# Optimization experiments

Hardware: AMD Instinct MI355X
Metric: run time of the kernel (lower is better)

## Reference

```python
import jax, jax.numpy as jnp
import numpy as np

N_NODES = 100000
N_EDGES = 3200000
DROP_P = 0.5


def gcn_conv(x, W, b, src, dst, deg_inv_sqrt, n):
    # PyG GCNConv with self-loops already folded into (src, dst):
    # out[j] = sum_{(i->j)} dinv[i]*dinv[j] * (x W)[i] + b
    h = x @ W
    norm = deg_inv_sqrt[src] * deg_inv_sqrt[dst]          # [E+N]
    msg = h[src] * norm[:, None]                          # [E+N, d_out]
    out = jax.ops.segment_sum(msg, dst, num_segments=n)
    return out + b


def dropout(x, key, p=DROP_P):
    keep = jax.random.bernoulli(key, 1.0 - p, x.shape)
    return jnp.where(keep, x / (1.0 - p), 0.0)


def setup_inputs() -> dict:
    key = jax.random.key(0)
    ks = jax.random.split(key, 8)
    x = jax.random.normal(ks[0], (N_NODES, 64), dtype=jnp.float32)
    edge_index = jax.random.randint(ks[1], (2, N_EDGES), 0, N_NODES, dtype=jnp.int64)
    def glorot(k, fin, fout):
        lim = float(np.sqrt(6.0 / (fin + fout)))
        return jax.random.uniform(k, (fin, fout), jnp.float32, -lim, lim)
    return {
        "x": x,
        "edge_index": edge_index,
        "W1": glorot(ks[2], 64, 32), "b1": jnp.zeros((32,), jnp.float32),
        "W2": glorot(ks[3], 32, 64), "b2": jnp.zeros((64,), jnp.float32),
        "W3": glorot(ks[4], 64, 32), "b3": jnp.zeros((32,), jnp.float32),
    }


def reference(x, edge_index, W1, b1, W2, b2, W3, b3):
    n = x.shape[0]
    loops = jnp.arange(n, dtype=edge_index.dtype)
    src = jnp.concatenate([edge_index[0], loops])          # [E+N]
    dst = jnp.concatenate([edge_index[1], loops])
    deg = jax.ops.segment_sum(jnp.ones_like(dst, dtype=x.dtype), dst, num_segments=n)
    deg_inv_sqrt = jnp.where(deg > 0, jax.lax.rsqrt(deg), 0.0)

    dkey = jax.random.key(42)
    k1, k2 = jax.random.split(dkey)

    h = gcn_conv(x, W1, b1, src, dst, deg_inv_sqrt, n)
    h = jax.nn.celu(h)
    h = dropout(h, k1)
    h = gcn_conv(h, W2, b2, src, dst, deg_inv_sqrt, n)
    h = jax.nn.celu(h)
    h = dropout(h, k2)
    h = gcn_conv(h, W3, b3, src, dst, deg_inv_sqrt, n)
    return jax.nn.celu(h)
```

## Files before the change

kernel.cpp:

```cpp
#include <hip/hip_runtime.h>
#include <stdint.h>
#include <stddef.h>

__host__ __device__ __forceinline__ uint32_t rotl32(uint32_t v, uint32_t r) {
  return (v << r) | (v >> (32u - r));
}

__host__ __device__ __forceinline__ void tf2x32(uint32_t k0, uint32_t k1,
                                                uint32_t x0, uint32_t x1,
                                                uint32_t& o0, uint32_t& o1) {
  uint32_t ks2 = k0 ^ k1 ^ 0x1BD11BDAu;
  x0 += k0; x1 += k1;
  x0 += x1; x1 = rotl32(x1, 13); x1 ^= x0;
  x0 += x1; x1 = rotl32(x1, 15); x1 ^= x0;
  x0 += x1; x1 = rotl32(x1, 26); x1 ^= x0;
  x0 += x1; x1 = rotl32(x1, 6);  x1 ^= x0;
  x0 += k1; x1 += ks2 + 1u;
  x0 += x1; x1 = rotl32(x1, 17); x1 ^= x0;
  x0 += x1; x1 = rotl32(x1, 29); x1 ^= x0;
  x0 += x1; x1 = rotl32(x1, 16); x1 ^= x0;
  x0 += x1; x1 = rotl32(x1, 24); x1 ^= x0;
  x0 += ks2; x1 += k0 + 2u;
  x0 += x1; x1 = rotl32(x1, 13); x1 ^= x0;
  x0 += x1; x1 = rotl32(x1, 15); x1 ^= x0;
  x0 += x1; x1 = rotl32(x1, 26); x1 ^= x0;
  x0 += x1; x1 = rotl32(x1, 6);  x1 ^= x0;
  x0 += k0; x1 += k1 + 3u;
  x0 += x1; x1 = rotl32(x1, 17); x1 ^= x0;
  x0 += x1; x1 = rotl32(x1, 29); x1 ^= x0;
  x0 += x1; x1 = rotl32(x1, 16); x1 ^= x0;
  x0 += x1; x1 = rotl32(x1, 24); x1 ^= x0;
  x0 += k1; x1 += ks2 + 4u;
  x0 += x1; x1 = rotl32(x1, 13); x1 ^= x0;
  x0 += x1; x1 = rotl32(x1, 15); x1 ^= x0;
  x0 += x1; x1 = rotl32(x1, 26); x1 ^= x0;
  x0 += x1; x1 = rotl32(x1, 6);  x1 ^= x0;
  x0 += ks2; x1 += k0 + 5u;
  o0 = x0; o1 = x1;
}

__device__ __forceinline__ bool tf_keep(uint32_t k0, uint32_t k1, uint32_t idx) {
  uint32_t o0, o1;
  tf2x32(k0, k1, 0u, idx, o0, o1);
  return ((o0 ^ o1) >> 31) == 0u;
}

#define CHUNK 4096
#define STASH 5120

__global__ __launch_bounds__(1024) void zero1024(uint32_t* __restrict__ p) {
  p[threadIdx.x] = 0u;
}

__global__ __launch_bounds__(256) void k1_hist(const int* __restrict__ dst,
                                               uint32_t* __restrict__ tbl,
                                               uint32_t* __restrict__ gbcnt,
                                               int E, int NB) {
  __shared__ uint32_t lc[1024];
  int tid = threadIdx.x;
  for (int i = tid; i < NB; i += 256) lc[i] = 0u;
  __syncthreads();
  int base = blockIdx.x * CHUNK;
  int end = min(base + CHUNK, E);
  for (int i = base + tid; i < end; i += 256)
    atomicAdd(&lc[((uint32_t)dst[i]) >> 7], 1u);
  __syncthreads();
  uint32_t* row = tbl + (size_t)blockIdx.x * NB;
  for (int i = tid; i < NB; i += 256) {
    uint32_t c = lc[i];
    row[i] = c;
    if (c) atomicAdd(&gbcnt[i], c);
  }
}

__global__ __launch_bounds__(1024) void k3_bscan(const uint32_t* __restrict__ gbcnt,
                                                 uint32_t* __restrict__ bbase, int NB) {
  __shared__ uint32_t s[1024];
  int i = threadIdx.x;
  uint32_t v = (i < NB) ? gbcnt[i] : 0u;
  s[i] = v;
  __syncthreads();
  for (int off = 1; off < 1024; off <<= 1) {
    uint32_t t = (i >= off) ? s[i - off] : 0u;
    __syncthreads();
    if (i >= off) s[i] += t;
    __syncthreads();
  }
  if (i < NB) bbase[i] = s[i] - v;
}

__global__ __launch_bounds__(256) void k4_bin(const int* __restrict__ src,
                                              const int* __restrict__ dst,
                                              uint32_t* __restrict__ tbl,
                                              uint32_t* __restrict__ staging,
                                              int E, int NB) {
  __shared__ uint32_t lcur[1024];
  __shared__ uint32_t ls[256];
  __shared__ uint32_t stage[CHUNK];
  int tid = threadIdx.x;
  uint32_t* row = tbl + (size_t)blockIdx.x * NB;
  uint32_t carry = 0u;
  for (int seg = 0; seg < 1024; seg += 256) {
    int i = seg + tid;
    uint32_t v = (i < NB) ? row[i] : 0u;
    ls[tid] = v;
    __syncthreads();
    for (int off = 1; off < 256; off <<= 1) {
      uint32_t t = (tid >= off) ? ls[tid - off] : 0u;
      __syncthreads();
      if (tid >= off) ls[tid] += t;
      __syncthreads();
    }
    uint32_t excl = carry + ls[tid] - v;
    if (i < NB) {
      row[i] = (excl << 16) | v;
      lcur[i] = excl;
    }
    carry += ls[255];
    __syncthreads();
  }
  int base = blockIdx.x * CHUNK;
  int end = min(base + CHUNK, E);
  for (int i = base + tid; i < end; i += 256) {
    uint32_t d = (uint32_t)dst[i];
    uint32_t b = d >> 7;
    uint32_t p = atomicAdd(&lcur[b], 1u);
    stage[p] = ((d & 127u) << 17) | (uint32_t)src[i];
  }
  __syncthreads();
  int cnt_total = end - base;
  uint32_t* outp = staging + (size_t)blockIdx.x * CHUNK;
  for (int i = tid; i < cnt_total; i += 256) outp[i] = stage[i];
}

__global__ __launch_bounds__(256) void k5_fin(
    const uint32_t* __restrict__ staging, const uint32_t* __restrict__ tbl,
    const uint32_t* __restrict__ bbase, uint32_t* __restrict__ rowp,
    float* __restrict__ dinv, uint32_t* __restrict__ esrc,
    int n, int E, int NBLK, int NB) {
  __shared__ uint32_t loff[1024];
  __shared__ uint32_t P[1025];
  __shared__ uint32_t ls[256];
  __shared__ uint32_t stash[STASH];
  __shared__ uint32_t lc[128];
  __shared__ uint32_t sc[128];
  __shared__ uint32_t lcur[128];
  int tid = threadIdx.x;
  int b = blockIdx.x;
  if (tid < 128) lc[tid] = 0u;
  uint32_t carry = 0u;
  for (int seg = 0; seg < 1024; seg += 256) {
    int i = seg + tid;
    uint32_t packed = (i < NBLK) ? tbl[(size_t)i * NB + b] : 0u;
    uint32_t v = packed & 0xFFFFu;
    if (i < 1024) loff[i] = packed >> 16;
    ls[tid] = v;
    __syncthreads();
    for (int off = 1; off < 256; off <<= 1) {
      uint32_t t = (tid >= off) ? ls[tid - off] : 0u;
      __syncthreads();
      if (tid >= off) ls[tid] += t;
      __syncthreads();
    }
    if (i < 1024) P[i] = carry + ls[tid] - v;
    carry += ls[255];
    __syncthreads();
  }
  if (tid == 0) P[NBLK] = carry;
  __syncthreads();
  uint32_t total = P[NBLK];
  for (uint32_t q = tid; q < total; q += 256) {
    int lo = 0, hi = NBLK;
    while (hi - lo > 1) {
      int mid = (lo + hi) >> 1;
      if (P[mid] <= q) lo = mid; else hi = mid;
    }
    uint32_t e = staging[(size_t)lo * CHUNK + loff[lo] + (q - P[lo])];
    if (q < STASH) stash[q] = e;
    atomicAdd(&lc[e >> 17], 1u);
  }
  __syncthreads();
  uint32_t myc = (tid < 128) ? lc[tid] : 0u;
  if (tid < 128) sc[tid] = myc;
  __syncthreads();
  for (int off = 1; off < 128; off <<= 1) {
    uint32_t t = (tid < 128 && tid >= off) ? sc[tid - off] : 0u;
    __syncthreads();
    if (tid < 128 && tid >= off) sc[tid] += t;
    __syncthreads();
  }
  uint32_t s = bbase[b];
  if (tid < 128) {
    uint32_t gstart = s + sc[tid] - myc;
    int node = (b << 7) + tid;
    if (node < n) {
      rowp[node] = gstart;
      dinv[node] = 1.0f / sqrtf((float)(myc + 1u));
    }
    lcur[tid] = gstart;
  }
  if (b == 0 && tid == 0) rowp[n] = (uint32_t)E;
  __syncthreads();
  for (uint32_t q = tid; q < total; q += 256) {
    uint32_t e;
    if (q < STASH) {
      e = stash[q];
    } else {
      int lo = 0, hi = NBLK;
      while (hi - lo > 1) {
        int mid = (lo + hi) >> 1;
        if (P[mid] <= q) lo = mid; else hi = mid;
      }
      e = staging[(size_t)lo * CHUNK + loff[lo] + (q - P[lo])];
    }
    uint32_t pos = atomicAdd(&lcur[e >> 17], 1u);
    esrc[pos] = e & 0x1FFFFu;
  }
}

__global__ __launch_bounds__(256) void gemm_n64_k32(
    const float* __restrict__ X, const float* __restrict__ W,
    const float* __restrict__ dinv, float* __restrict__ out, int n) {
  __shared__ float Ws[64 * 32];
  __shared__ float Xs[32 * 68];
  int tid = threadIdx.x;
  {
    const float4* Wv = (const float4*)W;
    float4* Wsv = (float4*)Ws;
    Wsv[tid] = Wv[tid];
    Wsv[tid + 256] = Wv[tid + 256];
  }
  int row0 = blockIdx.x * 32;
  {
    const float4* Xv = (const float4*)(X + (size_t)row0 * 64);
    int lim = (n - row0) * 16;
    float4 z = make_float4(0.f, 0.f, 0.f, 0.f);
    int i0 = tid, i1 = tid + 256;
    float4 v0 = (i0 < lim) ? Xv[i0] : z;
    float4 v1 = (i1 < lim) ? Xv[i1] : z;
    *(float4*)(Xs + (i0 >> 4) * 68 + ((i0 & 15) << 2)) = v0;
    *(float4*)(Xs + (i1 >> 4) * 68 + ((i1 & 15) << 2)) = v1;
  }
  __syncthreads();
  int r = tid >> 3;
  int c4 = (tid & 7) << 2;
  int row = row0 + r;
  if (row >= n) return;
  float4 acc = make_float4(0.f, 0.f, 0.f, 0.f);
#pragma unroll
  for (int k = 0; k < 64; k += 4) {
    float4 xv = *(const float4*)(Xs + r * 68 + k);
    float4 w0 = *(const float4*)(Ws + (k + 0) * 32 + c4);
    float4 w1 = *(const float4*)(Ws + (k + 1) * 32 + c4);
    float4 w2 = *(const float4*)(Ws + (k + 2) * 32 + c4);
    float4 w3 = *(const float4*)(Ws + (k + 3) * 32 + c4);
    acc.x = fmaf(xv.x, w0.x, acc.x); acc.y = fmaf(xv.x, w0.y, acc.y);
    acc.z = fmaf(xv.x, w0.z, acc.z); acc.w = fmaf(xv.x, w0.w, acc.w);
    acc.x = fmaf(xv.y, w1.x, acc.x); acc.y = fmaf(xv.y, w1.y, acc.y);
    acc.z = fmaf(xv.y, w1.z, acc.z); acc.w = fmaf(xv.y, w1.w, acc.w);
    acc.x = fmaf(xv.z, w2.x, acc.x); acc.y = fmaf(xv.z, w2.y, acc.y);
    acc.z = fmaf(xv.z, w2.z, acc.z); acc.w = fmaf(xv.z, w2.w, acc.w);
    acc.x = fmaf(xv.w, w3.x, acc.x); acc.y = fmaf(xv.w, w3.y, acc.y);
    acc.z = fmaf(xv.w, w3.z, acc.z); acc.w = fmaf(xv.w, w3.w, acc.w);
  }
  float dj = dinv[row];
  acc.x *= dj; acc.y *= dj; acc.z *= dj; acc.w *= dj;
  *(float4*)(out + (size_t)row * 32 + c4) = acc;
}

__global__ __launch_bounds__(256) void gemm_k32_n64_act(
    const float* __restrict__ X, const float* __restrict__ W,
    const float* __restrict__ bias, float* __restrict__ out,
    uint32_t k0, uint32_t k1, int n) {
  __shared__ float Ws[32 * 64];
  __shared__ float Xs[16 * 36];
  int tid = threadIdx.x;
  {
    const float4* Wv = (const float4*)W;
    float4* Wsv = (float4*)Ws;
    Wsv[tid] = Wv[tid];
    Wsv[tid + 256] = Wv[tid + 256];
  }
  int row0 = blockIdx.x * 16;
  if (tid < 128) {
    const float4* Xv = (const float4*)(X + (size_t)row0 * 32);
    int lim = (n - row0) * 8;
    float4 z = make_float4(0.f, 0.f, 0.f, 0.f);
    float4 v = (tid < lim) ? Xv[tid] : z;
    *(float4*)(Xs + (tid >> 3) * 36 + ((tid & 7) << 2)) = v;
  }
  __syncthreads();
  int r = tid >> 4;
  int c4 = (tid & 15) << 2;
  int row = row0 + r;
  if (row >= n) return;
  float4 acc = make_float4(0.f, 0.f, 0.f, 0.f);
#pragma unroll
  for (int k = 0; k < 32; k += 4) {
    float4 xv = *(const float4*)(Xs + r * 36 + k);
    float4 w0 = *(const float4*)(Ws + (k + 0) * 64 + c4);
    float4 w1 = *(const float4*)(Ws + (k + 1) * 64 + c4);
    float4 w2 = *(const float4*)(Ws + (k + 2) * 64 + c4);
    float4 w3 = *(const float4*)(Ws + (k + 3) * 64 + c4);
    acc.x = fmaf(xv.x, w0.x, acc.x); acc.y = fmaf(xv.x, w0.y, acc.y);
    acc.z = fmaf(xv.x, w0.z, acc.z); acc.w = fmaf(xv.x, w0.w, acc.w);
    acc.x = fmaf(xv.y, w1.x, acc.x); acc.y = fmaf(xv.y, w1.y, acc.y);
    acc.z = fmaf(xv.y, w1.z, acc.z); acc.w = fmaf(xv.y, w1.w, acc.w);
    acc.x = fmaf(xv.z, w2.x, acc.x); acc.y = fmaf(xv.z, w2.y, acc.y);
    acc.z = fmaf(xv.z, w2.z, acc.z); acc.w = fmaf(xv.z, w2.w, acc.w);
    acc.x = fmaf(xv.w, w3.x, acc.x); acc.y = fmaf(xv.w, w3.y, acc.y);
    acc.z = fmaf(xv.w, w3.z, acc.z); acc.w = fmaf(xv.w, w3.w, acc.w);
  }
  float4 bv = *(const float4*)(bias + c4);
  float vv[4] = {acc.x + bv.x, acc.y + bv.y, acc.z + bv.z, acc.w + bv.w};
  uint32_t base = (uint32_t)row * 64u + (uint32_t)c4;
#pragma unroll
  for (int q = 0; q < 4; ++q) {
    float v = vv[q];
    v = v > 0.f ? v : expm1f(v);
    vv[q] = tf_keep(k0, k1, base + q) ? v * 2.f : 0.f;
  }
  *(float4*)(out + (size_t)row * 64 + c4) = make_float4(vv[0], vv[1], vv[2], vv[3]);
}

__global__ __launch_bounds__(256) void gather_fin(
    const float* __restrict__ hs, const uint32_t* __restrict__ rowp,
    const uint32_t* __restrict__ esrc, const float* __restrict__ dinv,
    const float* __restrict__ bias, float* __restrict__ out,
    int n, int mode, uint32_t k0, uint32_t k1) {
  int gt = blockIdx.x * 256 + threadIdx.x;
  int j = gt >> 5;
  if (j >= n) return;
  int l = threadIdx.x & 31;
  int eslot = l >> 3;
  int c4 = (l & 7) << 2;
  float4 acc = make_float4(0.f, 0.f, 0.f, 0.f);
  uint32_t e1 = rowp[j + 1];
  uint32_t e = rowp[j] + (uint32_t)eslot;
  for (; e + 4 < e1; e += 8) {
    uint32_t s0 = esrc[e];
    uint32_t s1 = esrc[e + 4];
    float4 v0 = *(const float4*)(hs + ((size_t)s0 << 5) + c4);
    float4 v1 = *(const float4*)(hs + ((size_t)s1 << 5) + c4);
    acc.x += v0.x + v1.x;
    acc.y += v0.y + v1.y;
    acc.z += v0.z + v1.z;
    acc.w += v0.w + v1.w;
  }
  if (e < e1) {
    uint32_t s0 = esrc[e];
    float4 v0 = *(const float4*)(hs + ((size_t)s0 << 5) + c4);
    acc.x += v0.x; acc.y += v0.y; acc.z += v0.z; acc.w += v0.w;
  }
  acc.x += __shfl_xor(acc.x, 8);  acc.y += __shfl_xor(acc.y, 8);
  acc.z += __shfl_xor(acc.z, 8);  acc.w += __shfl_xor(acc.w, 8);
  acc.x += __shfl_xor(acc.x, 16); acc.y += __shfl_xor(acc.y, 16);
  acc.z += __shfl_xor(acc.z, 16); acc.w += __shfl_xor(acc.w, 16);
  int srcLane = (threadIdx.x & 32) | (l >> 2);
  float va = __shfl(acc.x, srcLane);
  float vb = __shfl(acc.y, srcLane);
  float vc = __shfl(acc.z, srcLane);
  float vd = __shfl(acc.w, srcLane);
  float lo = (l & 1) ? vb : va;
  float hi = (l & 1) ? vd : vc;
  float sum = (l & 2) ? hi : lo;
  sum += hs[gt];
  float dj = dinv[j];
  float v = dj * sum;
  if (mode == 1) {
    v += bias[l];
    v = v > 0.f ? v : expm1f(v);
  } else if (mode == 3) {
    v += bias[l];
    v = v > 0.f ? v : expm1f(v);
    v = tf_keep(k0, k1, (uint32_t)gt) ? v * 2.f : 0.f;
    v *= dj;
  }
  out[gt] = v;
}

extern "C" void kernel_launch(void* const* d_in, const int* in_sizes, int n_in,
                              void* d_out, int out_size, void* d_ws, size_t ws_size,
                              hipStream_t stream) {
  const float* x  = (const float*)d_in[0];
  const int*   ei = (const int*)d_in[1];
  const float* W1 = (const float*)d_in[2];
  const float* b1 = (const float*)d_in[3];
  const float* W2 = (const float*)d_in[4];
  const float* b2 = (const float*)d_in[5];
  const float* W3 = (const float*)d_in[6];
  const float* b3 = (const float*)d_in[7];
  float* out = (float*)d_out;

  const int n = in_sizes[0] / 64;
  const int E = in_sizes[1] / 2;
  const int* src = ei;
  const int* dst = ei + E;

  char* ws = (char*)d_ws;
  size_t off = 0;
  auto alloc = [&](size_t bytes) {
    void* p = ws + off;
    off = (off + bytes + 255) & ~(size_t)255;
    return p;
  };
  float*    A     = (float*)alloc((size_t)n * 32 * 4);
  float*    B     = (float*)alloc((size_t)n * 32 * 4);
  float*    C     = (float*)alloc((size_t)n * 64 * 4);
  float*    dinv  = (float*)alloc((size_t)n * 4);
  uint32_t* rowp  = (uint32_t*)alloc((size_t)(n + 1) * 4);
  uint32_t* esrc  = (uint32_t*)alloc((size_t)E * 4);
  uint32_t* gbcnt = (uint32_t*)alloc(1024 * 4);
  uint32_t* bbase = (uint32_t*)alloc(1024 * 4);
  uint32_t* staging = (uint32_t*)C;
  uint32_t* tbl     = (uint32_t*)A;
  (void)ws_size; (void)n_in; (void)out_size;

  uint32_t k1a, k1b, k2a, k2b;
  tf2x32(0u, 42u, 0u, 0u, k1a, k1b);
  tf2x32(0u, 42u, 0u, 1u, k2a, k2b);

  const int NB   = (n + 127) >> 7;
  const int NBLK = (E + CHUNK - 1) / CHUNK;
  const int nv   = n * 32;
  const int gV   = (nv + 255) / 256;
  const int gG1  = (n + 31) / 32;
  const int gG2  = (n + 15) / 16;
  dim3 blk(256);

  zero1024<<<1, dim3(1024), 0, stream>>>(gbcnt);
  k1_hist<<<NBLK, blk, 0, stream>>>(dst, tbl, gbcnt, E, NB);
  k3_bscan<<<1, dim3(1024), 0, stream>>>(gbcnt, bbase, NB);
  k4_bin<<<NBLK, blk, 0, stream>>>(src, dst, tbl, staging, E, NB);
  k5_fin<<<NB, blk, 0, stream>>>(staging, tbl, bbase, rowp, dinv, esrc, n, E, NBLK, NB);

  gemm_n64_k32<<<gG1, blk, 0, stream>>>(x, W1, dinv, A, n);
  gather_fin<<<gV, blk, 0, stream>>>(A, rowp, esrc, dinv, b1, B, n, 3, k1a, k1b);

  gather_fin<<<gV, blk, 0, stream>>>(B, rowp, esrc, dinv, nullptr, A, n, 0, 0u, 0u);
  gemm_k32_n64_act<<<gG2, blk, 0, stream>>>(A, W2, b2, C, k2a, k2b, n);

  gemm_n64_k32<<<gG1, blk, 0, stream>>>(C, W3, dinv, A, n);
  gather_fin<<<gV, blk, 0, stream>>>(A, rowp, esrc, dinv, b3, out, n, 1, 0u, 0u);
}
```

Measured before the change: 381.3 us.

## Fuse histogram and binning passes, drop binary search, cooperative index loads in gather

Merges the edge histogram and the binning kernel into one launch that keeps dst/src in registers, so the edge arrays are read once and one launch disappears. The CSR finalize kernel now walks each source block's run directly instead of binary-searching the prefix table per edge. The gather kernel loads 32 neighbour indices with one coalesced wavefront-wide read and broadcasts them by shuffle, instead of each lane reading indices separately. The trade-offs are higher register use in the fused kernel, and a per-thread serial run walk in finalize that can load-imbalance and lose coalescing.

```diff
diff --git a/kernel.cpp b/kernel.cpp
--- a/kernel.cpp
+++ b/kernel.cpp
@@ -52,25 +52,59 @@
   p[threadIdx.x] = 0u;
 }
 
-__global__ __launch_bounds__(256) void k1_hist(const int* __restrict__ dst,
-                                               uint32_t* __restrict__ tbl,
-                                               uint32_t* __restrict__ gbcnt,
-                                               int E, int NB) {
-  __shared__ uint32_t lc[1024];
+__global__ __launch_bounds__(256) void k4_binhist(const int* __restrict__ src,
+                                                  const int* __restrict__ dst,
+                                                  uint32_t* __restrict__ tbl,
+                                                  uint32_t* __restrict__ gbcnt,
+                                                  uint32_t* __restrict__ staging,
+                                                  int E, int NB) {
+  __shared__ uint32_t lcur[1024];
+  __shared__ uint32_t ls[256];
+  __shared__ uint32_t stage[CHUNK];
   int tid = threadIdx.x;
-  for (int i = tid; i < NB; i += 256) lc[i] = 0u;
+  for (int i = tid; i < NB; i += 256) lcur[i] = 0u;
   __syncthreads();
   int base = blockIdx.x * CHUNK;
   int end = min(base + CHUNK, E);
-  for (int i = base + tid; i < end; i += 256)
-    atomicAdd(&lc[((uint32_t)dst[i]) >> 7], 1u);
-  __syncthreads();
-  uint32_t* row = tbl + (size_t)blockIdx.x * NB;
-  for (int i = tid; i < NB; i += 256) {
-    uint32_t c = lc[i];
-    row[i] = c;
-    if (c) atomicAdd(&gbcnt[i], c);
-  }
+  uint32_t dv[16], sv[16];
+  int m = 0;
+  for (int i = base + tid; i < end; i += 256) {
+    dv[m] = (uint32_t)dst[i];
+    sv[m] = (uint32_t)src[i];
+    ++m;
+  }
+  for (int q = 0; q < m; ++q) atomicAdd(&lcur[dv[q] >> 7], 1u);
+  __syncthreads();
+  uint32_t carry = 0u;
+  for (int seg = 0; seg < 1024; seg += 256) {
+    int i = seg + tid;
+    uint32_t v = (i < NB) ? lcur[i] : 0u;
+    ls[tid] = v;
+    __syncthreads();
+    for (int off = 1; off < 256; off <<= 1) {
+      uint32_t t = (tid >= off) ? ls[tid - off] : 0u;
+      __syncthreads();
+      if (tid >= off) ls[tid] += t;
+      __syncthreads();
+    }
+    uint32_t excl = carry + ls[tid] - v;
+    if (i < NB) {
+      tbl[(size_t)blockIdx.x * NB + i] = (excl << 16) | v;
+      if (v) atomicAdd(&gbcnt[i], v);
+      lcur[i] = excl;
+    }
+    carry += ls[255];
+    __syncthreads();
+  }
+  for (int q = 0; q < m; ++q) {
+    uint32_t d = dv[q];
+    uint32_t p = atomicAdd(&lcur[d >> 7], 1u);
+    stage[p] = ((d & 127u) << 17) | sv[q];
+  }
+  __syncthreads();
+  int cnt_total = end - base;
+  uint32_t* outp = staging + (size_t)blockIdx.x * CHUNK;
+  for (int i = tid; i < cnt_total; i += 256) outp[i] = stage[i];
 }
 
 __global__ __launch_bounds__(1024) void k3_bscan(const uint32_t* __restrict__ gbcnt,
@@ -89,56 +123,12 @@
   if (i < NB) bbase[i] = s[i] - v;
 }
 
-__global__ __launch_bounds__(256) void k4_bin(const int* __restrict__ src,
-                                              const int* __restrict__ dst,
-                                              uint32_t* __restrict__ tbl,
-                                              uint32_t* __restrict__ staging,
-                                              int E, int NB) {
-  __shared__ uint32_t lcur[1024];
-  __shared__ uint32_t ls[256];
-  __shared__ uint32_t stage[CHUNK];
-  int tid = threadIdx.x;
-  uint32_t* row = tbl + (size_t)blockIdx.x * NB;
-  uint32_t carry = 0u;
-  for (int seg = 0; seg < 1024; seg += 256) {
-    int i = seg + tid;
-    uint32_t v = (i < NB) ? row[i] : 0u;
-    ls[tid] = v;
-    __syncthreads();
-    for (int off = 1; off < 256; off <<= 1) {
-      uint32_t t = (tid >= off) ? ls[tid - off] : 0u;
-      __syncthreads();
-      if (tid >= off) ls[tid] += t;
-      __syncthreads();
-    }
-    uint32_t excl = carry + ls[tid] - v;
-    if (i < NB) {
-      row[i] = (excl << 16) | v;
-      lcur[i] = excl;
-    }
-    carry += ls[255];
-    __syncthreads();
-  }
-  int base = blockIdx.x * CHUNK;
-  int end = min(base + CHUNK, E);
-  for (int i = base + tid; i < end; i += 256) {
-    uint32_t d = (uint32_t)dst[i];
-    uint32_t b = d >> 7;
-    uint32_t p = atomicAdd(&lcur[b], 1u);
-    stage[p] = ((d & 127u) << 17) | (uint32_t)src[i];
-  }
-  __syncthreads();
-  int cnt_total = end - base;
-  uint32_t* outp = staging + (size_t)blockIdx.x * CHUNK;
-  for (int i = tid; i < cnt_total; i += 256) outp[i] = stage[i];
-}
-
 __global__ __launch_bounds__(256) void k5_fin(
     const uint32_t* __restrict__ staging, const uint32_t* __restrict__ tbl,
     const uint32_t* __restrict__ bbase, uint32_t* __restrict__ rowp,
     float* __restrict__ dinv, uint32_t* __restrict__ esrc,
     int n, int E, int NBLK, int NB) {
-  __shared__ uint32_t loff[1024];
+  __shared__ uint32_t lpak[1024];
   __shared__ uint32_t P[1025];
   __shared__ uint32_t ls[256];
   __shared__ uint32_t stash[STASH];
@@ -152,8 +142,8 @@
   for (int seg = 0; seg < 1024; seg += 256) {
     int i = seg + tid;
     uint32_t packed = (i < NBLK) ? tbl[(size_t)i * NB + b] : 0u;
+    lpak[i] = packed;
     uint32_t v = packed & 0xFFFFu;
-    if (i < 1024) loff[i] = packed >> 16;
     ls[tid] = v;
     __syncthreads();
     for (int off = 1; off < 256; off <<= 1) {
@@ -162,22 +152,25 @@
       if (tid >= off) ls[tid] += t;
       __syncthreads();
     }
-    if (i < 1024) P[i] = carry + ls[tid] - v;
+    P[i] = carry + ls[tid] - v;
     carry += ls[255];
     __syncthreads();
   }
   if (tid == 0) P[NBLK] = carry;
   __syncthreads();
   uint32_t total = P[NBLK];
-  for (uint32_t q = tid; q < total; q += 256) {
-    int lo = 0, hi = NBLK;
-    while (hi - lo > 1) {
-      int mid = (lo + hi) >> 1;
-      if (P[mid] <= q) lo = mid; else hi = mid;
-    }
-    uint32_t e = staging[(size_t)lo * CHUNK + loff[lo] + (q - P[lo])];
-    if (q < STASH) stash[q] = e;
-    atomicAdd(&lc[e >> 17], 1u);
+  for (int i = tid; i < NBLK; i += 256) {
+    uint32_t packed = lpak[i];
+    uint32_t cnt = packed & 0xFFFFu;
+    uint32_t loff = packed >> 16;
+    uint32_t p = P[i];
+    const uint32_t* run = staging + (size_t)i * CHUNK + loff;
+    for (uint32_t t2 = 0; t2 < cnt; ++t2) {
+      uint32_t e = run[t2];
+      uint32_t q = p + t2;
+      if (q < STASH) stash[q] = e;
+      atomicAdd(&lc[e >> 17], 1u);
+    }
   }
   __syncthreads();
   uint32_t myc = (tid < 128) ? lc[tid] : 0u;
@@ -201,20 +194,28 @@
   }
   if (b == 0 && tid == 0) rowp[n] = (uint32_t)E;
   __syncthreads();
-  for (uint32_t q = tid; q < total; q += 256) {
-    uint32_t e;
-    if (q < STASH) {
-      e = stash[q];
-    } else {
-      int lo = 0, hi = NBLK;
-      while (hi - lo > 1) {
-        int mid = (lo + hi) >> 1;
-        if (P[mid] <= q) lo = mid; else hi = mid;
-      }
-      e = staging[(size_t)lo * CHUNK + loff[lo] + (q - P[lo])];
-    }
+  uint32_t lim = total < (uint32_t)STASH ? total : (uint32_t)STASH;
+  for (uint32_t q = tid; q < lim; q += 256) {
+    uint32_t e = stash[q];
     uint32_t pos = atomicAdd(&lcur[e >> 17], 1u);
     esrc[pos] = e & 0x1FFFFu;
+  }
+  if (total > (uint32_t)STASH) {
+    for (int i = tid; i < NBLK; i += 256) {
+      uint32_t packed = lpak[i];
+      uint32_t cnt = packed & 0xFFFFu;
+      uint32_t loff = packed >> 16;
+      uint32_t p = P[i];
+      const uint32_t* run = staging + (size_t)i * CHUNK + loff;
+      for (uint32_t t2 = 0; t2 < cnt; ++t2) {
+        uint32_t q = p + t2;
+        if (q >= (uint32_t)STASH) {
+          uint32_t e = run[t2];
+          uint32_t pos = atomicAdd(&lcur[e >> 17], 1u);
+          esrc[pos] = e & 0x1FFFFu;
+        }
+      }
+    }
   }
 }
 
@@ -335,22 +336,31 @@
   int eslot = l >> 3;
   int c4 = (l & 7) << 2;
   float4 acc = make_float4(0.f, 0.f, 0.f, 0.f);
-  uint32_t e1 = rowp[j + 1];
-  uint32_t e = rowp[j] + (uint32_t)eslot;
-  for (; e + 4 < e1; e += 8) {
-    uint32_t s0 = esrc[e];
-    uint32_t s1 = esrc[e + 4];
-    float4 v0 = *(const float4*)(hs + ((size_t)s0 << 5) + c4);
-    float4 v1 = *(const float4*)(hs + ((size_t)s1 << 5) + c4);
-    acc.x += v0.x + v1.x;
-    acc.y += v0.y + v1.y;
-    acc.z += v0.z + v1.z;
-    acc.w += v0.w + v1.w;
-  }
-  if (e < e1) {
-    uint32_t s0 = esrc[e];
-    float4 v0 = *(const float4*)(hs + ((size_t)s0 << 5) + c4);
-    acc.x += v0.x; acc.y += v0.y; acc.z += v0.z; acc.w += v0.w;
+  uint32_t e0 = rowp[j], e1 = rowp[j + 1];
+  uint32_t deg = e1 - e0;
+  uint32_t base = 0;
+  for (; base + 32 <= deg; base += 32) {
+    uint32_t idx = esrc[e0 + base + (uint32_t)l];
+#pragma unroll
+    for (int k = 0; k < 32; k += 4) {
+      uint32_t s = (uint32_t)__shfl((int)idx, k + eslot, 32);
+      const float4 v = *(const float4*)(hs + ((size_t)s << 5) + c4);
+      acc.x += v.x; acc.y += v.y; acc.z += v.z; acc.w += v.w;
+    }
+  }
+  if (base < deg) {
+    uint32_t rem = deg - base;
+    uint32_t li = (uint32_t)l < rem ? (uint32_t)l : rem - 1u;
+    uint32_t idx = esrc[e0 + base + li];
+    for (uint32_t k = 0; k < rem; k += 4) {
+      uint32_t kk = k + (uint32_t)eslot;
+      uint32_t ks = kk < rem ? kk : rem - 1u;
+      uint32_t s = (uint32_t)__shfl((int)idx, (int)ks, 32);
+      if (kk < rem) {
+        const float4 v = *(const float4*)(hs + ((size_t)s << 5) + c4);
+        acc.x += v.x; acc.y += v.y; acc.z += v.z; acc.w += v.w;
+      }
+    }
   }
   acc.x += __shfl_xor(acc.x, 8);  acc.y += __shfl_xor(acc.y, 8);
   acc.z += __shfl_xor(acc.z, 8);  acc.w += __shfl_xor(acc.w, 8);
@@ -429,9 +439,8 @@
   dim3 blk(256);
 
   zero1024<<<1, dim3(1024), 0, stream>>>(gbcnt);
-  k1_hist<<<NBLK, blk, 0, stream>>>(dst, tbl, gbcnt, E, NB);
+  k4_binhist<<<NBLK, blk, 0, stream>>>(src, dst, tbl, gbcnt, staging, E, NB);
   k3_bscan<<<1, dim3(1024), 0, stream>>>(gbcnt, bbase, NB);
-  k4_bin<<<NBLK, blk, 0, stream>>>(src, dst, tbl, staging, E, NB);
   k5_fin<<<NB, blk, 0, stream>>>(staging, tbl, bbase, rowp, dinv, esrc, n, E, NBLK, NB);
 
   gemm_n64_k32<<<gG1, blk, 0, stream>>>(x, W1, dinv, A, n);
```

New measurement: 376.0 us. Within noise of the previous version (-1.4%).
